# Optimization experiments

Measured on AMD Instinct MI355X. Metric: run time of the kernel, lower is better.

The kernel has to match this reference:

```python
import jax, jax.numpy as jnp
import numpy as np

DELTA_VAR = 0.5
DELTA_DIST = 2.0
ALPHA, BETA, GAMMA = 1.0, 1.0, 0.001
EPS = 1e-12  # guards sqrt(0) so vjp stays finite; forward effect negligible


def setup_inputs() -> dict:
    key = jax.random.key(0)
    k1, k2 = jax.random.split(key)
    N, E, H, W, C = 4, 16, 768, 768, 32
    input_ = jax.random.normal(k1, (N, E, H, W), dtype=jnp.float32)
    target = jax.random.randint(k2, (N, H, W), 0, C, dtype=jnp.int64)
    # guarantee labels are consecutive starting at 0 (every label present)
    target = target.at[:, 0, :C].set(jnp.arange(C, dtype=jnp.int64))
    return {"input_": input_, "target": target, "num_instances": C}


def _loss_single(emb, lab, C):
    # emb: [E,H,W], lab: [H,W] int
    E = emb.shape[0]
    emb_f = emb.reshape(E, -1).T          # [P,E]
    lab_f = lab.reshape(-1)               # [P]
    counts = jax.ops.segment_sum(jnp.ones(lab_f.shape, jnp.float32), lab_f, num_segments=C)  # [C]
    sums = jax.ops.segment_sum(emb_f, lab_f, num_segments=C)                                  # [C,E]
    means = sums / counts[:, None]        # cluster means, [C,E]

    # variance term: per-pixel distance to own cluster mean
    d = jnp.sqrt(jnp.maximum(jnp.sum((emb_f - means[lab_f]) ** 2, axis=1), EPS))  # [P]
    hinge = jnp.maximum(d - DELTA_VAR, 0.0) ** 2
    var_per_inst = jax.ops.segment_sum(hinge, lab_f, num_segments=C) / counts      # [C]
    variance_term = jnp.sum(var_per_inst) / C

    # distance term: pairwise hinged repulsion between cluster means
    diff = means[:, None, :] - means[None, :, :]                                   # [C,C,E]
    dist = jnp.sqrt(jnp.maximum(jnp.sum(diff ** 2, axis=2), EPS))                  # [C,C]
    repulsion = 2.0 * DELTA_DIST * (1.0 - jnp.eye(C, dtype=dist.dtype))
    hinged = jnp.maximum(repulsion - dist, 0.0) ** 2
    distance_term = jnp.sum(hinged) / (C * (C - 1))

    # regularizer: mean norm of cluster means
    reg_term = jnp.sum(jnp.sqrt(jnp.maximum(jnp.sum(means ** 2, axis=1), EPS))) / C

    return ALPHA * variance_term + BETA * distance_term + GAMMA * reg_term


def reference(input_, target, num_instances):
    C = int(num_instances)
    losses = jax.vmap(lambda e, l: _loss_single(e, l, C))(input_, target)  # [N]
    return jnp.sum(losses) / input_.shape[0]
```

## Files before the change

### kernel.cpp

```cpp
#include <hip/hip_runtime.h>
#include <stdint.h>

#define N_IMG 4
#define E_DIM 16
#define H_DIM 768
#define W_DIM 768
#define P_PIX (H_DIM * W_DIM)
#define C_CL 32

#define DELTA_VAR 0.5f
#define DELTA_DIST 2.0f
#define GAMMA_W 0.001f
#define EPS_F 1e-12f

#define WS_SUMS 0
#define WS_CNT 2048
#define WS_HINGE 2176
#define WS_HP 2176
#define WS_PART 4480
#define PART_STRIDE 544
#define NPART_FLOATS (N_IMG * 576 * PART_STRIDE)

#define P1_BLOCKS 576
#define P1_TILES 8

#define PX2 2048
#define BLOCKS2_X (P_PIX / PX2)

using bf16x8 = __attribute__((ext_vector_type(8))) short;
using f32x4 = __attribute__((ext_vector_type(4))) float;

__device__ __forceinline__ void gatomic_add(float* p, float v) {
#if defined(__HIP_DEVICE_COMPILE__)
  unsafeAtomicAdd(p, v);
#else
  atomicAdd(p, v);
#endif
}

__global__ __launch_bounds__(256) void pass1(const float* __restrict__ input,
                                             const int* __restrict__ target,
                                             float* __restrict__ ws,
                                             int partmode) {
  __shared__ float s_red[4][2][4][64];
  __shared__ float s_cnt[4][2][16];
  const int tid = threadIdx.x;
  const int wv = tid >> 6, l = tid & 63;
  const int g = l >> 4, cl = l & 15;
  const int n = blockIdx.y;

  const int wid = blockIdx.x * 4 + wv;
  const int base = wid * (P1_TILES * 32) + g * 8;
  const float* rowp = input + ((size_t)n * E_DIM + cl) * P_PIX;
  const int* tgt = target + (size_t)n * P_PIX;

  f32x4 acc0 = {0.f, 0.f, 0.f, 0.f}, acc1 = {0.f, 0.f, 0.f, 0.f};
  f32x4 cnt0 = {0.f, 0.f, 0.f, 0.f}, cnt1 = {0.f, 0.f, 0.f, 0.f};
  const short ONE = (short)0x3F80;
  const bf16x8 ones = {ONE, ONE, ONE, ONE, ONE, ONE, ONE, ONE};

  float4 va = *reinterpret_cast<const float4*>(rowp + base);
  float4 vb = *reinterpret_cast<const float4*>(rowp + base + 4);
  int4 la = *reinterpret_cast<const int4*>(tgt + base);
  int4 lb = *reinterpret_cast<const int4*>(tgt + base + 4);

  for (int t = 0; t < P1_TILES; ++t) {
    const float4 cva = va, cvb = vb;
    const int4 cla = la, clb = lb;
    if (t + 1 < P1_TILES) {
      const int p = base + (t + 1) * 32;
      va = *reinterpret_cast<const float4*>(rowp + p);
      vb = *reinterpret_cast<const float4*>(rowp + p + 4);
      la = *reinterpret_cast<const int4*>(tgt + p);
      lb = *reinterpret_cast<const int4*>(tgt + p + 4);
    }

    float ff[8];
    ff[0] = cva.x; ff[1] = cva.y; ff[2] = cva.z; ff[3] = cva.w;
    ff[4] = cvb.x; ff[5] = cvb.y; ff[6] = cvb.z; ff[7] = cvb.w;
    int lab[8];
    lab[0] = cla.x; lab[1] = cla.y; lab[2] = cla.z; lab[3] = cla.w;
    lab[4] = clb.x; lab[5] = clb.y; lab[6] = clb.z; lab[7] = clb.w;

    union BF { uint32_t w[4]; bf16x8 v; } Ahi, Alo, B0, B1;
#pragma unroll
    for (int q = 0; q < 4; ++q) {
      const uint32_t u0 = __float_as_uint(ff[2 * q]);
      const uint32_t u1 = __float_as_uint(ff[2 * q + 1]);
      Ahi.w[q] = (u0 >> 16) | (u1 & 0xFFFF0000u);
      const float r0 = ff[2 * q] - __uint_as_float(u0 & 0xFFFF0000u);
      const float r1 = ff[2 * q + 1] - __uint_as_float(u1 & 0xFFFF0000u);
      Alo.w[q] = (__float_as_uint(r0) >> 16) | (__float_as_uint(r1) & 0xFFFF0000u);
      B0.w[q] = ((lab[2 * q] == cl) ? 0x3F80u : 0u) |
                ((lab[2 * q + 1] == cl) ? 0x3F800000u : 0u);
      B1.w[q] = ((lab[2 * q] == cl + 16) ? 0x3F80u : 0u) |
                ((lab[2 * q + 1] == cl + 16) ? 0x3F800000u : 0u);
    }

    acc0 = __builtin_amdgcn_mfma_f32_16x16x32_bf16(Ahi.v, B0.v, acc0, 0, 0, 0);
    acc0 = __builtin_amdgcn_mfma_f32_16x16x32_bf16(Alo.v, B0.v, acc0, 0, 0, 0);
    acc1 = __builtin_amdgcn_mfma_f32_16x16x32_bf16(Ahi.v, B1.v, acc1, 0, 0, 0);
    acc1 = __builtin_amdgcn_mfma_f32_16x16x32_bf16(Alo.v, B1.v, acc1, 0, 0, 0);
    cnt0 = __builtin_amdgcn_mfma_f32_16x16x32_bf16(ones, B0.v, cnt0, 0, 0, 0);
    cnt1 = __builtin_amdgcn_mfma_f32_16x16x32_bf16(ones, B1.v, cnt1, 0, 0, 0);
  }

#pragma unroll
  for (int r = 0; r < 4; ++r) {
    s_red[wv][0][r][l] = acc0[r];
    s_red[wv][1][r][l] = acc1[r];
  }
  if (g == 0) {
    s_cnt[wv][0][cl] = cnt0[0];
    s_cnt[wv][1][cl] = cnt1[0];
  }
  __syncthreads();

  if (partmode) {
    float* pbase = ws + WS_PART +
                   (size_t)(n * P1_BLOCKS + blockIdx.x) * PART_STRIDE;
#pragma unroll
    for (int i = tid; i < 512; i += 256) {
      const int h = i >> 8, r = (i >> 6) & 3, ll = i & 63;
      const float v = s_red[0][h][r][ll] + s_red[1][h][r][ll] +
                      s_red[2][h][r][ll] + s_red[3][h][r][ll];
      const int c = (ll & 15) + 16 * h;
      const int e = (ll >> 4) * 4 + r;
      pbase[c * E_DIM + e] = v;
    }
    if (tid < C_CL) {
      const int h = tid >> 4, c16 = tid & 15;
      pbase[512 + tid] = s_cnt[0][h][c16] + s_cnt[1][h][c16] +
                         s_cnt[2][h][c16] + s_cnt[3][h][c16];
    }
  } else {
    float* gsum = ws + WS_SUMS + n * C_CL * E_DIM;
#pragma unroll
    for (int i = tid; i < 512; i += 256) {
      const int h = i >> 8, r = (i >> 6) & 3, ll = i & 63;
      const float v = s_red[0][h][r][ll] + s_red[1][h][r][ll] +
                      s_red[2][h][r][ll] + s_red[3][h][r][ll];
      const int c = (ll & 15) + 16 * h;
      const int e = (ll >> 4) * 4 + r;
      gatomic_add(&gsum[c * E_DIM + e], v);
    }
    if (tid < C_CL) {
      const int h = tid >> 4, c16 = tid & 15;
      const float v = s_cnt[0][h][c16] + s_cnt[1][h][c16] + s_cnt[2][h][c16] +
                      s_cnt[3][h][c16];
      gatomic_add(ws + WS_CNT + n * C_CL + tid, v);
    }
  }
}

__global__ __launch_bounds__(256) void reduce1(float* __restrict__ ws) {
  __shared__ float s[8][32];
  const int tid = threadIdx.x;
  const int bs = tid >> 5, il = tid & 31;
  const int n = blockIdx.y;
  const int i = blockIdx.x * 32 + il;
  const float* part = ws + WS_PART + (size_t)n * P1_BLOCKS * PART_STRIDE;
  float acc = 0.f;
#pragma unroll 8
  for (int b = bs; b < P1_BLOCKS; b += 8) acc += part[b * PART_STRIDE + i];
  s[bs][il] = acc;
  __syncthreads();
  if (tid < 32) {
    const int ii = blockIdx.x * 32 + tid;
    float t = s[0][tid] + s[1][tid] + s[2][tid] + s[3][tid] + s[4][tid] +
              s[5][tid] + s[6][tid] + s[7][tid];
    if (ii < 512)
      ws[WS_SUMS + n * 512 + ii] = t;
    else
      ws[WS_CNT + n * C_CL + (ii - 512)] = t;
  }
}

__global__ __launch_bounds__(256) void pass2(const float* __restrict__ input,
                                             const int* __restrict__ target,
                                             float* __restrict__ ws,
                                             int hmode) {
  __shared__ float s_meanT[E_DIM][C_CL];
  __shared__ float s_icnt[C_CL];
  __shared__ float s_part[4];
  const int tid = threadIdx.x;
  const int n = blockIdx.y;
  const float* gsum = ws + WS_SUMS + n * C_CL * E_DIM;
  const float* gcnt = ws + WS_CNT + n * C_CL;
  for (int i = tid; i < C_CL * E_DIM; i += 256) {
    const int c = i >> 4, e = i & 15;
    s_meanT[e][c] = gsum[i] / gcnt[c];
  }
  if (tid < C_CL) s_icnt[tid] = 1.0f / gcnt[tid];
  __syncthreads();

  const int pA = blockIdx.x * PX2 + tid * 4;
  const int pB = pA + 1024;
  const float* inp_n = input + (size_t)n * E_DIM * P_PIX;
  const int* tgt_n = target + (size_t)n * P_PIX;

  const int4 labA = *reinterpret_cast<const int4*>(tgt_n + pA);
  const int4 labB = *reinterpret_cast<const int4*>(tgt_n + pB);

  float aA0 = 0.f, aA1 = 0.f, aA2 = 0.f, aA3 = 0.f;
  float aB0 = 0.f, aB1 = 0.f, aB2 = 0.f, aB3 = 0.f;

#pragma unroll
  for (int e = 0; e < E_DIM; ++e) {
    const float* row = inp_n + (size_t)e * P_PIX;
    const float4 vA = *reinterpret_cast<const float4*>(row + pA);
    const float4 vB = *reinterpret_cast<const float4*>(row + pB);
    const float mA0 = s_meanT[e][labA.x];
    const float mA1 = s_meanT[e][labA.y];
    const float mA2 = s_meanT[e][labA.z];
    const float mA3 = s_meanT[e][labA.w];
    const float mB0 = s_meanT[e][labB.x];
    const float mB1 = s_meanT[e][labB.y];
    const float mB2 = s_meanT[e][labB.z];
    const float mB3 = s_meanT[e][labB.w];
    float d;
    d = vA.x - mA0; aA0 += d * d;
    d = vA.y - mA1; aA1 += d * d;
    d = vA.z - mA2; aA2 += d * d;
    d = vA.w - mA3; aA3 += d * d;
    d = vB.x - mB0; aB0 += d * d;
    d = vB.y - mB1; aB1 += d * d;
    d = vB.z - mB2; aB2 += d * d;
    d = vB.w - mB3; aB3 += d * d;
  }

  float dd, h, acc = 0.f;
  dd = sqrtf(fmaxf(aA0, EPS_F)); h = fmaxf(dd - DELTA_VAR, 0.f);
  acc += h * h * s_icnt[labA.x];
  dd = sqrtf(fmaxf(aA1, EPS_F)); h = fmaxf(dd - DELTA_VAR, 0.f);
  acc += h * h * s_icnt[labA.y];
  dd = sqrtf(fmaxf(aA2, EPS_F)); h = fmaxf(dd - DELTA_VAR, 0.f);
  acc += h * h * s_icnt[labA.z];
  dd = sqrtf(fmaxf(aA3, EPS_F)); h = fmaxf(dd - DELTA_VAR, 0.f);
  acc += h * h * s_icnt[labA.w];
  dd = sqrtf(fmaxf(aB0, EPS_F)); h = fmaxf(dd - DELTA_VAR, 0.f);
  acc += h * h * s_icnt[labB.x];
  dd = sqrtf(fmaxf(aB1, EPS_F)); h = fmaxf(dd - DELTA_VAR, 0.f);
  acc += h * h * s_icnt[labB.y];
  dd = sqrtf(fmaxf(aB2, EPS_F)); h = fmaxf(dd - DELTA_VAR, 0.f);
  acc += h * h * s_icnt[labB.z];
  dd = sqrtf(fmaxf(aB3, EPS_F)); h = fmaxf(dd - DELTA_VAR, 0.f);
  acc += h * h * s_icnt[labB.w];

#pragma unroll
  for (int off = 32; off > 0; off >>= 1) acc += __shfl_down(acc, off);
  if ((tid & 63) == 0) s_part[tid >> 6] = acc;
  __syncthreads();
  if (tid == 0) {
    const float total = s_part[0] + s_part[1] + s_part[2] + s_part[3];
    if (hmode)
      ws[WS_HP + n * BLOCKS2_X + blockIdx.x] = total;
    else
      gatomic_add(ws + WS_HINGE + n, total);
  }
}

__global__ __launch_bounds__(256) void finalize(const float* __restrict__ ws,
                                                float* __restrict__ out,
                                                int hmode) {
  __shared__ float s_mean[N_IMG * C_CL * E_DIM];
  __shared__ float red[256];
  const int tid = threadIdx.x;
  for (int i = tid; i < N_IMG * C_CL * E_DIM; i += 256) {
    s_mean[i] = ws[WS_SUMS + i] / ws[WS_CNT + (i >> 4)];
  }
  __syncthreads();

  float acc = 0.f;
  if (hmode) {
    for (int i = tid; i < N_IMG * BLOCKS2_X; i += 256)
      acc += ws[WS_HP + i] * (1.0f / C_CL);
  } else {
    if (tid < N_IMG) acc += ws[WS_HINGE + tid] * (1.0f / C_CL);
  }
  for (int i = tid; i < N_IMG * C_CL; i += 256) {
    float nrm2 = 0.f;
    const float* m = s_mean + i * E_DIM;
#pragma unroll
    for (int e = 0; e < E_DIM; ++e) nrm2 += m[e] * m[e];
    acc += GAMMA_W * sqrtf(fmaxf(nrm2, EPS_F)) * (1.0f / C_CL);
  }
  for (int t = tid; t < N_IMG * C_CL * C_CL; t += 256) {
    const int n = t / (C_CL * C_CL);
    const int r = t - n * C_CL * C_CL;
    const int a = r >> 5, b = r & 31;
    if (a != b) {
      const float* ma = s_mean + (n * C_CL + a) * E_DIM;
      const float* mb = s_mean + (n * C_CL + b) * E_DIM;
      float d2 = 0.f;
#pragma unroll
      for (int e = 0; e < E_DIM; ++e) {
        const float df = ma[e] - mb[e];
        d2 += df * df;
      }
      const float dist = sqrtf(fmaxf(d2, EPS_F));
      const float hd = fmaxf(2.f * DELTA_DIST - dist, 0.f);
      acc += hd * hd * (1.0f / (C_CL * (C_CL - 1)));
    }
  }

  red[tid] = acc;
  __syncthreads();
  for (int s = 128; s > 0; s >>= 1) {
    if (tid < s) red[tid] += red[tid + s];
    __syncthreads();
  }
  if (tid == 0) out[0] = red[0] * (1.0f / N_IMG);
}

extern "C" void kernel_launch(void* const* d_in, const int* in_sizes, int n_in,
                              void* d_out, int out_size, void* d_ws,
                              size_t ws_size, hipStream_t stream) {
  const float* input = (const float*)d_in[0];
  const int* target = (const int*)d_in[1];
  float* ws = (float*)d_ws;
  float* out = (float*)d_out;

  const bool big_ws = ws_size >= (size_t)(WS_PART + NPART_FLOATS) * 4;
  const bool mid_ws = ws_size >= (size_t)WS_PART * 4;
  const int partmode = big_ws ? 1 : 0;
  const int hmode = mid_ws ? 1 : 0;

  if (!big_ws || !mid_ws) {
    hipMemsetAsync(ws, 0, 2180 * sizeof(float), stream);
  }
  dim3 grid1(P1_BLOCKS, N_IMG);
  pass1<<<grid1, 256, 0, stream>>>(input, target, ws, partmode);
  if (big_ws) {
    dim3 gridr(17, N_IMG);
    reduce1<<<gridr, 256, 0, stream>>>(ws);
  }
  dim3 grid2(BLOCKS2_X, N_IMG);
  pass2<<<grid2, 256, 0, stream>>>(input, target, ws, hmode);
  finalize<<<1, 256, 0, stream>>>(ws, out, hmode);
}
```

Measured before the change: 259.5 us.

## Fuse all passes into one cooperative kernel with grid-wide syncs

Result: slower. 809.0 us (+211.8%).

```diff
diff --git a/kernel.cpp b/kernel.cpp
--- a/kernel.cpp
+++ b/kernel.cpp
@@ -1,5 +1,8 @@
 #include <hip/hip_runtime.h>
+#include <hip/hip_cooperative_groups.h>
 #include <stdint.h>
+
+namespace cg = cooperative_groups;
 
 #define N_IMG 4
 #define E_DIM 16
@@ -19,13 +22,16 @@
 #define WS_HP 2176
 #define WS_PART 4480
 #define PART_STRIDE 544
-#define NPART_FLOATS (N_IMG * 576 * PART_STRIDE)
+
+#define FB_PER_IMG 256
+#define F_TILES 18
+#define NPART_F (N_IMG * FB_PER_IMG * PART_STRIDE)
 
 #define P1_BLOCKS 576
 #define P1_TILES 8
-
 #define PX2 2048
 #define BLOCKS2_X (P_PIX / PX2)
+#define NPART_L (N_IMG * P1_BLOCKS * PART_STRIDE)
 
 using bf16x8 = __attribute__((ext_vector_type(8))) short;
 using f32x4 = __attribute__((ext_vector_type(4))) float;
@@ -36,6 +42,266 @@
 #else
   atomicAdd(p, v);
 #endif
+}
+
+__global__ __launch_bounds__(256, 4) void fused(const float* __restrict__ input,
+                                                const int* __restrict__ target,
+                                                float* __restrict__ ws,
+                                                float* __restrict__ out) {
+  __shared__ float s_red[4][2][4][64];
+  __shared__ float s_cnt[4][2][16];
+  __shared__ float s_r8[8][32];
+  __shared__ float s_meanT[E_DIM][C_CL];
+  __shared__ float s_icnt[C_CL];
+  __shared__ float s_part[4];
+  __shared__ float s_fm[N_IMG * C_CL * E_DIM];
+  __shared__ float s_red2[256];
+
+  const int tid = threadIdx.x;
+  const int bid = blockIdx.x;
+  const int n = bid >> 8, blk = bid & 255;
+
+  {
+    const int wv = tid >> 6, l = tid & 63;
+    const int g = l >> 4, cl = l & 15;
+    const int wid = blk * 4 + wv;
+    const int base = wid * 576 + g * 8;
+    const float* rowp = input + ((size_t)n * E_DIM + cl) * P_PIX;
+    const int* tgt = target + (size_t)n * P_PIX;
+
+    f32x4 acc0 = {0.f, 0.f, 0.f, 0.f}, acc1 = {0.f, 0.f, 0.f, 0.f};
+    f32x4 cnt0 = {0.f, 0.f, 0.f, 0.f}, cnt1 = {0.f, 0.f, 0.f, 0.f};
+    const short ONE = (short)0x3F80;
+    const bf16x8 ones = {ONE, ONE, ONE, ONE, ONE, ONE, ONE, ONE};
+
+    float4 va = *reinterpret_cast<const float4*>(rowp + base);
+    float4 vb = *reinterpret_cast<const float4*>(rowp + base + 4);
+    int4 la = *reinterpret_cast<const int4*>(tgt + base);
+    int4 lb = *reinterpret_cast<const int4*>(tgt + base + 4);
+
+    for (int t = 0; t < F_TILES; ++t) {
+      const float4 cva = va, cvb = vb;
+      const int4 cla = la, clb = lb;
+      if (t + 1 < F_TILES) {
+        const int p = base + (t + 1) * 32;
+        va = *reinterpret_cast<const float4*>(rowp + p);
+        vb = *reinterpret_cast<const float4*>(rowp + p + 4);
+        la = *reinterpret_cast<const int4*>(tgt + p);
+        lb = *reinterpret_cast<const int4*>(tgt + p + 4);
+      }
+      float ff[8];
+      ff[0] = cva.x; ff[1] = cva.y; ff[2] = cva.z; ff[3] = cva.w;
+      ff[4] = cvb.x; ff[5] = cvb.y; ff[6] = cvb.z; ff[7] = cvb.w;
+      int lab[8];
+      lab[0] = cla.x; lab[1] = cla.y; lab[2] = cla.z; lab[3] = cla.w;
+      lab[4] = clb.x; lab[5] = clb.y; lab[6] = clb.z; lab[7] = clb.w;
+
+      union BF { uint32_t w[4]; bf16x8 v; } Ahi, Alo, B0, B1;
+#pragma unroll
+      for (int q = 0; q < 4; ++q) {
+        const uint32_t u0 = __float_as_uint(ff[2 * q]);
+        const uint32_t u1 = __float_as_uint(ff[2 * q + 1]);
+        Ahi.w[q] = (u0 >> 16) | (u1 & 0xFFFF0000u);
+        const float r0 = ff[2 * q] - __uint_as_float(u0 & 0xFFFF0000u);
+        const float r1 = ff[2 * q + 1] - __uint_as_float(u1 & 0xFFFF0000u);
+        Alo.w[q] = (__float_as_uint(r0) >> 16) | (__float_as_uint(r1) & 0xFFFF0000u);
+        B0.w[q] = ((lab[2 * q] == cl) ? 0x3F80u : 0u) |
+                  ((lab[2 * q + 1] == cl) ? 0x3F800000u : 0u);
+        B1.w[q] = ((lab[2 * q] == cl + 16) ? 0x3F80u : 0u) |
+                  ((lab[2 * q + 1] == cl + 16) ? 0x3F800000u : 0u);
+      }
+      acc0 = __builtin_amdgcn_mfma_f32_16x16x32_bf16(Ahi.v, B0.v, acc0, 0, 0, 0);
+      acc0 = __builtin_amdgcn_mfma_f32_16x16x32_bf16(Alo.v, B0.v, acc0, 0, 0, 0);
+      acc1 = __builtin_amdgcn_mfma_f32_16x16x32_bf16(Ahi.v, B1.v, acc1, 0, 0, 0);
+      acc1 = __builtin_amdgcn_mfma_f32_16x16x32_bf16(Alo.v, B1.v, acc1, 0, 0, 0);
+      cnt0 = __builtin_amdgcn_mfma_f32_16x16x32_bf16(ones, B0.v, cnt0, 0, 0, 0);
+      cnt1 = __builtin_amdgcn_mfma_f32_16x16x32_bf16(ones, B1.v, cnt1, 0, 0, 0);
+    }
+
+#pragma unroll
+    for (int r = 0; r < 4; ++r) {
+      s_red[wv][0][r][l] = acc0[r];
+      s_red[wv][1][r][l] = acc1[r];
+    }
+    if (g == 0) {
+      s_cnt[wv][0][cl] = cnt0[0];
+      s_cnt[wv][1][cl] = cnt1[0];
+    }
+    __syncthreads();
+
+    float* pbase = ws + WS_PART + (size_t)(n * FB_PER_IMG + blk) * PART_STRIDE;
+#pragma unroll
+    for (int i = tid; i < 512; i += 256) {
+      const int h = i >> 8, r = (i >> 6) & 3, ll = i & 63;
+      const float v = s_red[0][h][r][ll] + s_red[1][h][r][ll] +
+                      s_red[2][h][r][ll] + s_red[3][h][r][ll];
+      const int c = (ll & 15) + 16 * h;
+      const int e = (ll >> 4) * 4 + r;
+      pbase[c * E_DIM + e] = v;
+    }
+    if (tid < C_CL) {
+      const int h = tid >> 4, c16 = tid & 15;
+      pbase[512 + tid] = s_cnt[0][h][c16] + s_cnt[1][h][c16] +
+                         s_cnt[2][h][c16] + s_cnt[3][h][c16];
+    }
+  }
+  __threadfence();
+  cg::this_grid().sync();
+
+  if (bid < 68) {
+    const int nn = bid / 17, ib = bid - nn * 17;
+    const int bs = tid >> 5, il = tid & 31;
+    const int i = ib * 32 + il;
+    const float* part = ws + WS_PART + (size_t)nn * FB_PER_IMG * PART_STRIDE;
+    float acc = 0.f;
+#pragma unroll 8
+    for (int b = bs; b < FB_PER_IMG; b += 8) acc += part[b * PART_STRIDE + i];
+    s_r8[bs][il] = acc;
+    __syncthreads();
+    if (tid < 32) {
+      const int ii = ib * 32 + tid;
+      float t = s_r8[0][tid] + s_r8[1][tid] + s_r8[2][tid] + s_r8[3][tid] +
+                s_r8[4][tid] + s_r8[5][tid] + s_r8[6][tid] + s_r8[7][tid];
+      if (ii < 512)
+        ws[WS_SUMS + nn * 512 + ii] = t;
+      else
+        ws[WS_CNT + nn * C_CL + (ii - 512)] = t;
+    }
+  }
+  __threadfence();
+  cg::this_grid().sync();
+
+  {
+    const float* gsum = ws + WS_SUMS + n * 512;
+    const float* gcnt = ws + WS_CNT + n * C_CL;
+    for (int i = tid; i < 512; i += 256) {
+      const int c = i >> 4, e = i & 15;
+      s_meanT[e][c] = gsum[i] / gcnt[c];
+    }
+    if (tid < C_CL) s_icnt[tid] = 1.0f / gcnt[tid];
+    __syncthreads();
+
+    const int base2 = blk * 2304;
+    const float* inp_n = input + (size_t)n * E_DIM * P_PIX;
+    const int* tgt_n = target + (size_t)n * P_PIX;
+    float acc = 0.f;
+
+    {
+      const int pA = base2 + tid * 4;
+      const int pB = pA + 1024;
+      const int4 labA = *reinterpret_cast<const int4*>(tgt_n + pA);
+      const int4 labB = *reinterpret_cast<const int4*>(tgt_n + pB);
+      float aA0 = 0.f, aA1 = 0.f, aA2 = 0.f, aA3 = 0.f;
+      float aB0 = 0.f, aB1 = 0.f, aB2 = 0.f, aB3 = 0.f;
+#pragma unroll
+      for (int e = 0; e < E_DIM; ++e) {
+        const float* row = inp_n + (size_t)e * P_PIX;
+        const float4 vA = *reinterpret_cast<const float4*>(row + pA);
+        const float4 vB = *reinterpret_cast<const float4*>(row + pB);
+        float d;
+        d = vA.x - s_meanT[e][labA.x]; aA0 += d * d;
+        d = vA.y - s_meanT[e][labA.y]; aA1 += d * d;
+        d = vA.z - s_meanT[e][labA.z]; aA2 += d * d;
+        d = vA.w - s_meanT[e][labA.w]; aA3 += d * d;
+        d = vB.x - s_meanT[e][labB.x]; aB0 += d * d;
+        d = vB.y - s_meanT[e][labB.y]; aB1 += d * d;
+        d = vB.z - s_meanT[e][labB.z]; aB2 += d * d;
+        d = vB.w - s_meanT[e][labB.w]; aB3 += d * d;
+      }
+      float dd, h;
+      dd = sqrtf(fmaxf(aA0, EPS_F)); h = fmaxf(dd - DELTA_VAR, 0.f);
+      acc += h * h * s_icnt[labA.x];
+      dd = sqrtf(fmaxf(aA1, EPS_F)); h = fmaxf(dd - DELTA_VAR, 0.f);
+      acc += h * h * s_icnt[labA.y];
+      dd = sqrtf(fmaxf(aA2, EPS_F)); h = fmaxf(dd - DELTA_VAR, 0.f);
+      acc += h * h * s_icnt[labA.z];
+      dd = sqrtf(fmaxf(aA3, EPS_F)); h = fmaxf(dd - DELTA_VAR, 0.f);
+      acc += h * h * s_icnt[labA.w];
+      dd = sqrtf(fmaxf(aB0, EPS_F)); h = fmaxf(dd - DELTA_VAR, 0.f);
+      acc += h * h * s_icnt[labB.x];
+      dd = sqrtf(fmaxf(aB1, EPS_F)); h = fmaxf(dd - DELTA_VAR, 0.f);
+      acc += h * h * s_icnt[labB.y];
+      dd = sqrtf(fmaxf(aB2, EPS_F)); h = fmaxf(dd - DELTA_VAR, 0.f);
+      acc += h * h * s_icnt[labB.z];
+      dd = sqrtf(fmaxf(aB3, EPS_F)); h = fmaxf(dd - DELTA_VAR, 0.f);
+      acc += h * h * s_icnt[labB.w];
+    }
+    if (tid < 64) {
+      const int pT = base2 + 2048 + tid * 4;
+      const int4 lab = *reinterpret_cast<const int4*>(tgt_n + pT);
+      float a0 = 0.f, a1 = 0.f, a2 = 0.f, a3 = 0.f;
+#pragma unroll
+      for (int e = 0; e < E_DIM; ++e) {
+        const float* row = inp_n + (size_t)e * P_PIX;
+        const float4 v = *reinterpret_cast<const float4*>(row + pT);
+        float d;
+        d = v.x - s_meanT[e][lab.x]; a0 += d * d;
+        d = v.y - s_meanT[e][lab.y]; a1 += d * d;
+        d = v.z - s_meanT[e][lab.z]; a2 += d * d;
+        d = v.w - s_meanT[e][lab.w]; a3 += d * d;
+      }
+      float dd, h;
+      dd = sqrtf(fmaxf(a0, EPS_F)); h = fmaxf(dd - DELTA_VAR, 0.f);
+      acc += h * h * s_icnt[lab.x];
+      dd = sqrtf(fmaxf(a1, EPS_F)); h = fmaxf(dd - DELTA_VAR, 0.f);
+      acc += h * h * s_icnt[lab.y];
+      dd = sqrtf(fmaxf(a2, EPS_F)); h = fmaxf(dd - DELTA_VAR, 0.f);
+      acc += h * h * s_icnt[lab.z];
+      dd = sqrtf(fmaxf(a3, EPS_F)); h = fmaxf(dd - DELTA_VAR, 0.f);
+      acc += h * h * s_icnt[lab.w];
+    }
+#pragma unroll
+    for (int off = 32; off > 0; off >>= 1) acc += __shfl_down(acc, off);
+    if ((tid & 63) == 0) s_part[tid >> 6] = acc;
+    __syncthreads();
+    if (tid == 0)
+      ws[WS_HP + n * FB_PER_IMG + blk] =
+          s_part[0] + s_part[1] + s_part[2] + s_part[3];
+  }
+  __threadfence();
+  cg::this_grid().sync();
+
+  if (bid == 0) {
+    for (int i = tid; i < N_IMG * C_CL * E_DIM; i += 256) {
+      s_fm[i] = ws[WS_SUMS + i] / ws[WS_CNT + (i >> 4)];
+    }
+    __syncthreads();
+    float acc = 0.f;
+    for (int i = tid; i < N_IMG * FB_PER_IMG; i += 256)
+      acc += ws[WS_HP + i] * (1.0f / C_CL);
+    for (int i = tid; i < N_IMG * C_CL; i += 256) {
+      float nrm2 = 0.f;
+      const float* m = s_fm + i * E_DIM;
+#pragma unroll
+      for (int e = 0; e < E_DIM; ++e) nrm2 += m[e] * m[e];
+      acc += GAMMA_W * sqrtf(fmaxf(nrm2, EPS_F)) * (1.0f / C_CL);
+    }
+    for (int t = tid; t < N_IMG * C_CL * C_CL; t += 256) {
+      const int nn = t / (C_CL * C_CL);
+      const int r = t - nn * C_CL * C_CL;
+      const int a = r >> 5, b = r & 31;
+      if (a != b) {
+        const float* ma = s_fm + (nn * C_CL + a) * E_DIM;
+        const float* mb = s_fm + (nn * C_CL + b) * E_DIM;
+        float d2 = 0.f;
+#pragma unroll
+        for (int e = 0; e < E_DIM; ++e) {
+          const float df = ma[e] - mb[e];
+          d2 += df * df;
+        }
+        const float dist = sqrtf(fmaxf(d2, EPS_F));
+        const float hd = fmaxf(2.f * DELTA_DIST - dist, 0.f);
+        acc += hd * hd * (1.0f / (C_CL * (C_CL - 1)));
+      }
+    }
+    s_red2[tid] = acc;
+    __syncthreads();
+    for (int s = 128; s > 0; s >>= 1) {
+      if (tid < s) s_red2[tid] += s_red2[tid + s];
+      __syncthreads();
+    }
+    if (tid == 0) out[0] = s_red2[0] * (1.0f / N_IMG);
+  }
 }
 
 __global__ __launch_bounds__(256) void pass1(const float* __restrict__ input,
@@ -48,7 +314,6 @@
   const int wv = tid >> 6, l = tid & 63;
   const int g = l >> 4, cl = l & 15;
   const int n = blockIdx.y;
-
   const int wid = blockIdx.x * 4 + wv;
   const int base = wid * (P1_TILES * 32) + g * 8;
   const float* rowp = input + ((size_t)n * E_DIM + cl) * P_PIX;
@@ -74,14 +339,12 @@
       la = *reinterpret_cast<const int4*>(tgt + p);
       lb = *reinterpret_cast<const int4*>(tgt + p + 4);
     }
-
     float ff[8];
     ff[0] = cva.x; ff[1] = cva.y; ff[2] = cva.z; ff[3] = cva.w;
     ff[4] = cvb.x; ff[5] = cvb.y; ff[6] = cvb.z; ff[7] = cvb.w;
     int lab[8];
     lab[0] = cla.x; lab[1] = cla.y; lab[2] = cla.z; lab[3] = cla.w;
     lab[4] = clb.x; lab[5] = clb.y; lab[6] = clb.z; lab[7] = clb.w;
-
     union BF { uint32_t w[4]; bf16x8 v; } Ahi, Alo, B0, B1;
 #pragma unroll
     for (int q = 0; q < 4; ++q) {
@@ -96,7 +359,6 @@
       B1.w[q] = ((lab[2 * q] == cl + 16) ? 0x3F80u : 0u) |
                 ((lab[2 * q + 1] == cl + 16) ? 0x3F800000u : 0u);
     }
-
     acc0 = __builtin_amdgcn_mfma_f32_16x16x32_bf16(Ahi.v, B0.v, acc0, 0, 0, 0);
     acc0 = __builtin_amdgcn_mfma_f32_16x16x32_bf16(Alo.v, B0.v, acc0, 0, 0, 0);
     acc1 = __builtin_amdgcn_mfma_f32_16x16x32_bf16(Ahi.v, B1.v, acc1, 0, 0, 0);
@@ -198,37 +460,25 @@
   const int pB = pA + 1024;
   const float* inp_n = input + (size_t)n * E_DIM * P_PIX;
   const int* tgt_n = target + (size_t)n * P_PIX;
-
   const int4 labA = *reinterpret_cast<const int4*>(tgt_n + pA);
   const int4 labB = *reinterpret_cast<const int4*>(tgt_n + pB);
-
   float aA0 = 0.f, aA1 = 0.f, aA2 = 0.f, aA3 = 0.f;
   float aB0 = 0.f, aB1 = 0.f, aB2 = 0.f, aB3 = 0.f;
-
 #pragma unroll
   for (int e = 0; e < E_DIM; ++e) {
     const float* row = inp_n + (size_t)e * P_PIX;
     const float4 vA = *reinterpret_cast<const float4*>(row + pA);
     const float4 vB = *reinterpret_cast<const float4*>(row + pB);
-    const float mA0 = s_meanT[e][labA.x];
-    const float mA1 = s_meanT[e][labA.y];
-    const float mA2 = s_meanT[e][labA.z];
-    const float mA3 = s_meanT[e][labA.w];
-    const float mB0 = s_meanT[e][labB.x];
-    const float mB1 = s_meanT[e][labB.y];
-    const float mB2 = s_meanT[e][labB.z];
-    const float mB3 = s_meanT[e][labB.w];
     float d;
-    d = vA.x - mA0; aA0 += d * d;
-    d = vA.y - mA1; aA1 += d * d;
-    d = vA.z - mA2; aA2 += d * d;
-    d = vA.w - mA3; aA3 += d * d;
-    d = vB.x - mB0; aB0 += d * d;
-    d = vB.y - mB1; aB1 += d * d;
-    d = vB.z - mB2; aB2 += d * d;
-    d = vB.w - mB3; aB3 += d * d;
-  }
-
+    d = vA.x - s_meanT[e][labA.x]; aA0 += d * d;
+    d = vA.y - s_meanT[e][labA.y]; aA1 += d * d;
+    d = vA.z - s_meanT[e][labA.z]; aA2 += d * d;
+    d = vA.w - s_meanT[e][labA.w]; aA3 += d * d;
+    d = vB.x - s_meanT[e][labB.x]; aB0 += d * d;
+    d = vB.y - s_meanT[e][labB.y]; aB1 += d * d;
+    d = vB.z - s_meanT[e][labB.z]; aB2 += d * d;
+    d = vB.w - s_meanT[e][labB.w]; aB3 += d * d;
+  }
   float dd, h, acc = 0.f;
   dd = sqrtf(fmaxf(aA0, EPS_F)); h = fmaxf(dd - DELTA_VAR, 0.f);
   acc += h * h * s_icnt[labA.x];
@@ -246,7 +496,6 @@
   acc += h * h * s_icnt[labB.z];
   dd = sqrtf(fmaxf(aB3, EPS_F)); h = fmaxf(dd - DELTA_VAR, 0.f);
   acc += h * h * s_icnt[labB.w];
-
 #pragma unroll
   for (int off = 32; off > 0; off >>= 1) acc += __shfl_down(acc, off);
   if ((tid & 63) == 0) s_part[tid >> 6] = acc;
@@ -270,7 +519,6 @@
     s_mean[i] = ws[WS_SUMS + i] / ws[WS_CNT + (i >> 4)];
   }
   __syncthreads();
-
   float acc = 0.f;
   if (hmode) {
     for (int i = tid; i < N_IMG * BLOCKS2_X; i += 256)
@@ -303,7 +551,6 @@
       acc += hd * hd * (1.0f / (C_CL * (C_CL - 1)));
     }
   }
-
   red[tid] = acc;
   __syncthreads();
   for (int s = 128; s > 0; s >>= 1) {
@@ -321,11 +568,17 @@
   float* ws = (float*)d_ws;
   float* out = (float*)d_out;
 
-  const bool big_ws = ws_size >= (size_t)(WS_PART + NPART_FLOATS) * 4;
+  if (ws_size >= (size_t)(WS_PART + NPART_F) * 4) {
+    void* args[] = {(void*)&input, (void*)&target, (void*)&ws, (void*)&out};
+    hipError_t err = hipLaunchCooperativeKernel(
+        (void*)fused, dim3(N_IMG * FB_PER_IMG), dim3(256), args, 0, stream);
+    if (err == hipSuccess) return;
+  }
+
+  const bool big_ws = ws_size >= (size_t)(WS_PART + NPART_L) * 4;
   const bool mid_ws = ws_size >= (size_t)WS_PART * 4;
   const int partmode = big_ws ? 1 : 0;
   const int hmode = mid_ws ? 1 : 0;
-
   if (!big_ws || !mid_ws) {
     hipMemsetAsync(ws, 0, 2180 * sizeof(float), stream);
   }
```

## Stage pass1 embedding tiles through LDS with coalesced wide loads

Applied to the files above, without the earlier changes.

Result: slower. 274.5 us (+5.8%).

```diff
diff --git a/kernel.cpp b/kernel.cpp
--- a/kernel.cpp
+++ b/kernel.cpp
@@ -19,10 +19,11 @@
 #define WS_HP 2176
 #define WS_PART 4480
 #define PART_STRIDE 544
-#define NPART_FLOATS (N_IMG * 576 * PART_STRIDE)
-
-#define P1_BLOCKS 576
-#define P1_TILES 8
+#define P1_BLOCKS 288
+#define NPART_L (N_IMG * P1_BLOCKS * PART_STRIDE)
+
+#define P1_ROUNDS 2
+#define STG 260
 
 #define PX2 2048
 #define BLOCKS2_X (P_PIX / PX2)
@@ -42,6 +43,8 @@
                                              const int* __restrict__ target,
                                              float* __restrict__ ws,
                                              int partmode) {
+  __shared__ float s_stage[4][16 * STG];
+  __shared__ int s_ltab[4][STG];
   __shared__ float s_red[4][2][4][64];
   __shared__ float s_cnt[4][2][16];
   const int tid = threadIdx.x;
@@ -50,8 +53,8 @@
   const int n = blockIdx.y;
 
   const int wid = blockIdx.x * 4 + wv;
-  const int base = wid * (P1_TILES * 32) + g * 8;
-  const float* rowp = input + ((size_t)n * E_DIM + cl) * P_PIX;
+  const int wave_base = wid * 512;
+  const float* inp_n = input + (size_t)n * E_DIM * P_PIX;
   const int* tgt = target + (size_t)n * P_PIX;
 
   f32x4 acc0 = {0.f, 0.f, 0.f, 0.f}, acc1 = {0.f, 0.f, 0.f, 0.f};
@@ -59,50 +62,57 @@
   const short ONE = (short)0x3F80;
   const bf16x8 ones = {ONE, ONE, ONE, ONE, ONE, ONE, ONE, ONE};
 
-  float4 va = *reinterpret_cast<const float4*>(rowp + base);
-  float4 vb = *reinterpret_cast<const float4*>(rowp + base + 4);
-  int4 la = *reinterpret_cast<const int4*>(tgt + base);
-  int4 lb = *reinterpret_cast<const int4*>(tgt + base + 4);
-
-  for (int t = 0; t < P1_TILES; ++t) {
-    const float4 cva = va, cvb = vb;
-    const int4 cla = la, clb = lb;
-    if (t + 1 < P1_TILES) {
-      const int p = base + (t + 1) * 32;
-      va = *reinterpret_cast<const float4*>(rowp + p);
-      vb = *reinterpret_cast<const float4*>(rowp + p + 4);
-      la = *reinterpret_cast<const int4*>(tgt + p);
-      lb = *reinterpret_cast<const int4*>(tgt + p + 4);
-    }
-
-    float ff[8];
-    ff[0] = cva.x; ff[1] = cva.y; ff[2] = cva.z; ff[3] = cva.w;
-    ff[4] = cvb.x; ff[5] = cvb.y; ff[6] = cvb.z; ff[7] = cvb.w;
-    int lab[8];
-    lab[0] = cla.x; lab[1] = cla.y; lab[2] = cla.z; lab[3] = cla.w;
-    lab[4] = clb.x; lab[5] = clb.y; lab[6] = clb.z; lab[7] = clb.w;
-
-    union BF { uint32_t w[4]; bf16x8 v; } Ahi, Alo, B0, B1;
-#pragma unroll
-    for (int q = 0; q < 4; ++q) {
-      const uint32_t u0 = __float_as_uint(ff[2 * q]);
-      const uint32_t u1 = __float_as_uint(ff[2 * q + 1]);
-      Ahi.w[q] = (u0 >> 16) | (u1 & 0xFFFF0000u);
-      const float r0 = ff[2 * q] - __uint_as_float(u0 & 0xFFFF0000u);
-      const float r1 = ff[2 * q + 1] - __uint_as_float(u1 & 0xFFFF0000u);
-      Alo.w[q] = (__float_as_uint(r0) >> 16) | (__float_as_uint(r1) & 0xFFFF0000u);
-      B0.w[q] = ((lab[2 * q] == cl) ? 0x3F80u : 0u) |
-                ((lab[2 * q + 1] == cl) ? 0x3F800000u : 0u);
-      B1.w[q] = ((lab[2 * q] == cl + 16) ? 0x3F80u : 0u) |
-                ((lab[2 * q + 1] == cl + 16) ? 0x3F800000u : 0u);
-    }
-
-    acc0 = __builtin_amdgcn_mfma_f32_16x16x32_bf16(Ahi.v, B0.v, acc0, 0, 0, 0);
-    acc0 = __builtin_amdgcn_mfma_f32_16x16x32_bf16(Alo.v, B0.v, acc0, 0, 0, 0);
-    acc1 = __builtin_amdgcn_mfma_f32_16x16x32_bf16(Ahi.v, B1.v, acc1, 0, 0, 0);
-    acc1 = __builtin_amdgcn_mfma_f32_16x16x32_bf16(Alo.v, B1.v, acc1, 0, 0, 0);
-    cnt0 = __builtin_amdgcn_mfma_f32_16x16x32_bf16(ones, B0.v, cnt0, 0, 0, 0);
-    cnt1 = __builtin_amdgcn_mfma_f32_16x16x32_bf16(ones, B1.v, cnt1, 0, 0, 0);
+  for (int r = 0; r < P1_ROUNDS; ++r) {
+    const int rbase = wave_base + r * 256;
+    float4 stg[16];
+#pragma unroll
+    for (int p = 0; p < 16; ++p)
+      stg[p] = *reinterpret_cast<const float4*>(inp_n + (size_t)p * P_PIX +
+                                                rbase + l * 4);
+    const int4 stl = *reinterpret_cast<const int4*>(tgt + rbase + l * 4);
+#pragma unroll
+    for (int p = 0; p < 16; ++p)
+      *reinterpret_cast<float4*>(&s_stage[wv][p * STG + l * 4]) = stg[p];
+    *reinterpret_cast<int4*>(&s_ltab[wv][l * 4]) = stl;
+
+    for (int t = 0; t < 8; ++t) {
+      const int off = t * 32 + g * 8;
+      const float4 cva =
+          *reinterpret_cast<const float4*>(&s_stage[wv][cl * STG + off]);
+      const float4 cvb =
+          *reinterpret_cast<const float4*>(&s_stage[wv][cl * STG + off + 4]);
+      const int4 cla = *reinterpret_cast<const int4*>(&s_ltab[wv][off]);
+      const int4 clb = *reinterpret_cast<const int4*>(&s_ltab[wv][off + 4]);
+
+      float ff[8];
+      ff[0] = cva.x; ff[1] = cva.y; ff[2] = cva.z; ff[3] = cva.w;
+      ff[4] = cvb.x; ff[5] = cvb.y; ff[6] = cvb.z; ff[7] = cvb.w;
+      int lab[8];
+      lab[0] = cla.x; lab[1] = cla.y; lab[2] = cla.z; lab[3] = cla.w;
+      lab[4] = clb.x; lab[5] = clb.y; lab[6] = clb.z; lab[7] = clb.w;
+
+      union BF { uint32_t w[4]; bf16x8 v; } Ahi, Alo, B0, B1;
+#pragma unroll
+      for (int q = 0; q < 4; ++q) {
+        const uint32_t u0 = __float_as_uint(ff[2 * q]);
+        const uint32_t u1 = __float_as_uint(ff[2 * q + 1]);
+        Ahi.w[q] = (u0 >> 16) | (u1 & 0xFFFF0000u);
+        const float r0 = ff[2 * q] - __uint_as_float(u0 & 0xFFFF0000u);
+        const float r1 = ff[2 * q + 1] - __uint_as_float(u1 & 0xFFFF0000u);
+        Alo.w[q] =
+            (__float_as_uint(r0) >> 16) | (__float_as_uint(r1) & 0xFFFF0000u);
+        B0.w[q] = ((lab[2 * q] == cl) ? 0x3F80u : 0u) |
+                  ((lab[2 * q + 1] == cl) ? 0x3F800000u : 0u);
+        B1.w[q] = ((lab[2 * q] == cl + 16) ? 0x3F80u : 0u) |
+                  ((lab[2 * q + 1] == cl + 16) ? 0x3F800000u : 0u);
+      }
+      acc0 = __builtin_amdgcn_mfma_f32_16x16x32_bf16(Ahi.v, B0.v, acc0, 0, 0, 0);
+      acc0 = __builtin_amdgcn_mfma_f32_16x16x32_bf16(Alo.v, B0.v, acc0, 0, 0, 0);
+      acc1 = __builtin_amdgcn_mfma_f32_16x16x32_bf16(Ahi.v, B1.v, acc1, 0, 0, 0);
+      acc1 = __builtin_amdgcn_mfma_f32_16x16x32_bf16(Alo.v, B1.v, acc1, 0, 0, 0);
+      cnt0 = __builtin_amdgcn_mfma_f32_16x16x32_bf16(ones, B0.v, cnt0, 0, 0, 0);
+      cnt1 = __builtin_amdgcn_mfma_f32_16x16x32_bf16(ones, B1.v, cnt1, 0, 0, 0);
+    }
   }
 
 #pragma unroll
@@ -198,37 +208,25 @@
   const int pB = pA + 1024;
   const float* inp_n = input + (size_t)n * E_DIM * P_PIX;
   const int* tgt_n = target + (size_t)n * P_PIX;
-
   const int4 labA = *reinterpret_cast<const int4*>(tgt_n + pA);
   const int4 labB = *reinterpret_cast<const int4*>(tgt_n + pB);
-
   float aA0 = 0.f, aA1 = 0.f, aA2 = 0.f, aA3 = 0.f;
   float aB0 = 0.f, aB1 = 0.f, aB2 = 0.f, aB3 = 0.f;
-
 #pragma unroll
   for (int e = 0; e < E_DIM; ++e) {
     const float* row = inp_n + (size_t)e * P_PIX;
     const float4 vA = *reinterpret_cast<const float4*>(row + pA);
     const float4 vB = *reinterpret_cast<const float4*>(row + pB);
-    const float mA0 = s_meanT[e][labA.x];
-    const float mA1 = s_meanT[e][labA.y];
-    const float mA2 = s_meanT[e][labA.z];
-    const float mA3 = s_meanT[e][labA.w];
-    const float mB0 = s_meanT[e][labB.x];
-    const float mB1 = s_meanT[e][labB.y];
-    const float mB2 = s_meanT[e][labB.z];
-    const float mB3 = s_meanT[e][labB.w];
     float d;
-    d = vA.x - mA0; aA0 += d * d;
-    d = vA.y - mA1; aA1 += d * d;
-    d = vA.z - mA2; aA2 += d * d;
-    d = vA.w - mA3; aA3 += d * d;
-    d = vB.x - mB0; aB0 += d * d;
-    d = vB.y - mB1; aB1 += d * d;
-    d = vB.z - mB2; aB2 += d * d;
-    d = vB.w - mB3; aB3 += d * d;
-  }
-
+    d = vA.x - s_meanT[e][labA.x]; aA0 += d * d;
+    d = vA.y - s_meanT[e][labA.y]; aA1 += d * d;
+    d = vA.z - s_meanT[e][labA.z]; aA2 += d * d;
+    d = vA.w - s_meanT[e][labA.w]; aA3 += d * d;
+    d = vB.x - s_meanT[e][labB.x]; aB0 += d * d;
+    d = vB.y - s_meanT[e][labB.y]; aB1 += d * d;
+    d = vB.z - s_meanT[e][labB.z]; aB2 += d * d;
+    d = vB.w - s_meanT[e][labB.w]; aB3 += d * d;
+  }
   float dd, h, acc = 0.f;
   dd = sqrtf(fmaxf(aA0, EPS_F)); h = fmaxf(dd - DELTA_VAR, 0.f);
   acc += h * h * s_icnt[labA.x];
@@ -246,7 +244,6 @@
   acc += h * h * s_icnt[labB.z];
   dd = sqrtf(fmaxf(aB3, EPS_F)); h = fmaxf(dd - DELTA_VAR, 0.f);
   acc += h * h * s_icnt[labB.w];
-
 #pragma unroll
   for (int off = 32; off > 0; off >>= 1) acc += __shfl_down(acc, off);
   if ((tid & 63) == 0) s_part[tid >> 6] = acc;
@@ -270,7 +267,6 @@
     s_mean[i] = ws[WS_SUMS + i] / ws[WS_CNT + (i >> 4)];
   }
   __syncthreads();
-
   float acc = 0.f;
   if (hmode) {
     for (int i = tid; i < N_IMG * BLOCKS2_X; i += 256)
@@ -303,7 +299,6 @@
       acc += hd * hd * (1.0f / (C_CL * (C_CL - 1)));
     }
   }
-
   red[tid] = acc;
   __syncthreads();
   for (int s = 128; s > 0; s >>= 1) {
@@ -321,11 +316,10 @@
   float* ws = (float*)d_ws;
   float* out = (float*)d_out;
 
-  const bool big_ws = ws_size >= (size_t)(WS_PART + NPART_FLOATS) * 4;
+  const bool big_ws = ws_size >= (size_t)(WS_PART + NPART_L) * 4;
   const bool mid_ws = ws_size >= (size_t)WS_PART * 4;
   const int partmode = big_ws ? 1 : 0;
   const int hmode = mid_ws ? 1 : 0;
-
   if (!big_ws || !mid_ws) {
     hipMemsetAsync(ws, 0, 2180 * sizeof(float), stream);
   }
```
